# Performance work log

Hardware: AMD Instinct MI355X
Metric: run time of the kernel (lower is better)

Reference implementation:

```python
import jax, jax.numpy as jnp
import numpy as np

B, SQ, SP, H = 4, 2048, 2048, 256


def setup_inputs() -> dict:
    key = jax.random.key(0)
    k1, k2, k3 = jax.random.split(key, 3)
    return {
        "encode_input1": jax.random.normal(k1, (B, SQ, H), jnp.float32),  # E_q
        "encode_input2": jax.random.normal(k2, (B, SP, H), jnp.float32),  # E_p
        "input1_mask": jnp.ones((B, SP), jnp.float32),  # mask over seq_p (dim 1 of U)
        "input2_mask": jnp.ones((B, SQ), jnp.float32),  # mask over seq_q (dim 2 of U)
        "W": jax.random.normal(k3, (3 * H,), jnp.float32) * (1.0 / np.sqrt(3 * H)),
    }


def reference(encode_input1, encode_input2, input1_mask, input2_mask, W):
    E_q, E_p = encode_input1, encode_input2  # [B,q,H], [B,p,H]
    h = W.shape[0] // 3
    w_q, w_p, w_m = W[:h], W[h:2 * h], W[2 * h:]
    # Trilinear decomposition of Linear(cat([E_q, E_p, E_q*E_p])) -> [B,p,q]
    sq = E_q @ w_q                                   # [B,q]
    sp = E_p @ w_p                                   # [B,p]
    tri = jnp.einsum('bph,bqh->bpq', E_p * w_m, E_q)  # [B,p,q]
    U = sp[:, :, None] + sq[:, None, :] + tri
    mask = input1_mask[:, :, None] * input2_mask[:, None, :]  # [B,p,q]
    U = jnp.where(mask < 0.5, jnp.float32(-1e9), U)
    A_p = jax.nn.softmax(U, axis=2)  # softmax over q
    B_p = jax.nn.softmax(U, axis=1)  # softmax over p
    A1 = jnp.einsum('bpq,bqh->bph', A_p, E_q)  # A''_p  [B,p,H]
    B1 = jnp.einsum('bpq,bph->bqh', B_p, E_p)  # B''_p  [B,q,H]
    A2 = jnp.einsum('bpq,bqh->bph', A_p, B1)   # A'''_p [B,p,H]
    B2 = jnp.einsum('bpq,bph->bqh', B_p, A1)   # B'''_p [B,q,H]
    G_q_p = jnp.concatenate([E_p, A1, A2, E_p * A1, E_p * A2], axis=-1)  # [B,p,5H]
    G_p_q = jnp.concatenate([E_q, B1, B2, E_q * B1, E_q * B2], axis=-1)  # [B,q,5H]
    return (G_p_q, G_q_p)
```

## Files before the change

### kernel.cpp

```cpp
#include <hip/hip_runtime.h>
#include <math.h>

#define BB 4
#define SS 2048
#define HH 256
#define NEG_BIG -1e9f
#define GSEG ((size_t)BB * SS * 5 * HH)
#define NT ((size_t)BB * SS * HH)

typedef unsigned short ushort_t;
typedef __attribute__((ext_vector_type(8))) __bf16 bf16x8;
typedef __attribute__((ext_vector_type(8))) unsigned short ushort8;
typedef __attribute__((ext_vector_type(4))) float f32x4;

__device__ __forceinline__ void bsplit(float x, ushort_t& hi, ushort_t& lo) {
  union { float f; unsigned u; } a; a.f = x;
  unsigned r = a.u + 0x7FFFu + ((a.u >> 16) & 1u);
  ushort_t h = (ushort_t)(r >> 16);
  union { unsigned u; float f; } hf; hf.u = ((unsigned)h) << 16;
  float l = x - hf.f;
  union { float f; unsigned u; } b; b.f = l;
  unsigned r2 = b.u + 0x7FFFu + ((b.u >> 16) & 1u);
  hi = h; lo = (ushort_t)(r2 >> 16);
}

__global__ __launch_bounds__(256) void k_rowdots(
    const float* __restrict__ Eq, const float* __restrict__ Ep,
    const float* __restrict__ W,
    float* __restrict__ sqv, float* __restrict__ spv) {
  int g = blockIdx.x * 256 + threadIdx.x;
  int wid = g >> 6;
  int lane = g & 63;
  const int total = BB * SS;
  int isp = wid >= total;
  int row = isp ? (wid - total) : wid;
  const float* Er = (isp ? Ep : Eq) + (size_t)row * HH;
  const float* w = W + (isp ? HH : 0);
  float4 e = ((const float4*)Er)[lane];
  float4 wv = ((const float4*)w)[lane];
  float acc = e.x * wv.x + e.y * wv.y + e.z * wv.z + e.w * wv.w;
#pragma unroll
  for (int off = 32; off > 0; off >>= 1) acc += __shfl_down(acc, off, 64);
  if (lane == 0) (isp ? spv : sqv)[row] = acc;
}

__global__ __launch_bounds__(256) void k_tc(
    const float* __restrict__ src, ushort_t* __restrict__ dhi, ushort_t* __restrict__ dlo) {
  __shared__ float tile[64][65];
  int b = blockIdx.z;
  int r0 = blockIdx.x << 6;
  int h0 = blockIdx.y << 6;
  int tid = threadIdx.x;
  int rl = tid >> 4, c4 = (tid & 15) << 2;
  size_t srcb = (size_t)b * SS * HH;
#pragma unroll
  for (int i = 0; i < 4; ++i) {
    float4 v = *(const float4*)(src + srcb + (size_t)(r0 + rl + 16 * i) * HH + h0 + c4);
    tile[rl + 16 * i][c4 + 0] = v.x;
    tile[rl + 16 * i][c4 + 1] = v.y;
    tile[rl + 16 * i][c4 + 2] = v.z;
    tile[rl + 16 * i][c4 + 3] = v.w;
  }
  __syncthreads();
  size_t dstb = (size_t)b * HH;
#pragma unroll
  for (int i = 0; i < 4; ++i) {
    int h = rl + 16 * i;
    ushort4 h4, l4;
    ushort_t hh, ll;
    bsplit(tile[c4 + 0][h], hh, ll); h4.x = hh; l4.x = ll;
    bsplit(tile[c4 + 1][h], hh, ll); h4.y = hh; l4.y = ll;
    bsplit(tile[c4 + 2][h], hh, ll); h4.z = hh; l4.z = ll;
    bsplit(tile[c4 + 3][h], hh, ll); h4.w = hh; l4.w = ll;
    size_t o = (dstb + h0 + h) * SS + r0 + c4;
    *(ushort4*)(dhi + o) = h4;
    *(ushort4*)(dlo + o) = l4;
  }
}

__global__ __launch_bounds__(256) void k_tri(
    const float* __restrict__ Eq, const float* __restrict__ Ep,
    const float* __restrict__ W,
    const float* __restrict__ m1, const float* __restrict__ m2,
    const float* __restrict__ spv, const float* __restrict__ sqv,
    float* __restrict__ U) {
  alignas(16) __shared__ float As[32][68];
  alignas(16) __shared__ float Bs[32][68];
  int b = blockIdx.z;
  int q0 = blockIdx.x << 6;
  int p0 = blockIdx.y << 6;
  int tid = threadIdx.x;
  int tx = tid & 15, ty = tid >> 4;
  size_t bS = (size_t)b * SS;
  const float* EpB = Ep + bS * HH;
  const float* EqB = Eq + bS * HH;
  const float* wm = W + 2 * HH;
  float acc[4][4] = {};
  for (int k0 = 0; k0 < HH; k0 += 32) {
#pragma unroll
    for (int i = 0; i < 2; ++i) {
      int idx = tid + i * 256;
      int r = idx >> 3;
      int c4 = (idx & 7) << 2;
      float4 w4 = *(const float4*)(wm + k0 + c4);
      float4 a4 = *(const float4*)(EpB + (size_t)(p0 + r) * HH + k0 + c4);
      float4 b4 = *(const float4*)(EqB + (size_t)(q0 + r) * HH + k0 + c4);
      As[c4 + 0][r] = a4.x * w4.x;
      As[c4 + 1][r] = a4.y * w4.y;
      As[c4 + 2][r] = a4.z * w4.z;
      As[c4 + 3][r] = a4.w * w4.w;
      Bs[c4 + 0][r] = b4.x;
      Bs[c4 + 1][r] = b4.y;
      Bs[c4 + 2][r] = b4.z;
      Bs[c4 + 3][r] = b4.w;
    }
    __syncthreads();
#pragma unroll
    for (int k = 0; k < 32; ++k) {
      float4 a4 = *(const float4*)&As[k][ty << 2];
      float4 b4 = *(const float4*)&Bs[k][tx << 2];
      acc[0][0] += a4.x * b4.x; acc[0][1] += a4.x * b4.y; acc[0][2] += a4.x * b4.z; acc[0][3] += a4.x * b4.w;
      acc[1][0] += a4.y * b4.x; acc[1][1] += a4.y * b4.y; acc[1][2] += a4.y * b4.z; acc[1][3] += a4.y * b4.w;
      acc[2][0] += a4.z * b4.x; acc[2][1] += a4.z * b4.y; acc[2][2] += a4.z * b4.z; acc[2][3] += a4.z * b4.w;
      acc[3][0] += a4.w * b4.x; acc[3][1] += a4.w * b4.y; acc[3][2] += a4.w * b4.z; acc[3][3] += a4.w * b4.w;
    }
    __syncthreads();
  }
  int prow = p0 + (ty << 2);
  int qcol = q0 + (tx << 2);
  float spr[4], mpr[4], sqc[4], mqc[4];
#pragma unroll
  for (int i = 0; i < 4; ++i) { spr[i] = spv[bS + prow + i]; mpr[i] = m1[bS + prow + i]; }
#pragma unroll
  for (int j = 0; j < 4; ++j) { sqc[j] = sqv[bS + qcol + j]; mqc[j] = m2[bS + qcol + j]; }
#pragma unroll
  for (int i = 0; i < 4; ++i) {
    float4 o;
    o.x = (mpr[i] * mqc[0] < 0.5f) ? NEG_BIG : (acc[i][0] + spr[i] + sqc[0]);
    o.y = (mpr[i] * mqc[1] < 0.5f) ? NEG_BIG : (acc[i][1] + spr[i] + sqc[1]);
    o.z = (mpr[i] * mqc[2] < 0.5f) ? NEG_BIG : (acc[i][2] + spr[i] + sqc[2]);
    o.w = (mpr[i] * mqc[3] < 0.5f) ? NEG_BIG : (acc[i][3] + spr[i] + sqc[3]);
    *(float4*)(U + (bS + prow + i) * SS + qcol) = o;
  }
}

__global__ __launch_bounds__(256) void k_rowstats(
    const float* __restrict__ U, float* __restrict__ rowmax, float* __restrict__ rowinv) {
  __shared__ float redm[4];
  __shared__ float reds[4];
  int row = blockIdx.x;
  int tid = threadIdx.x;
  const float* u = U + (size_t)row * SS;
  float4 v1 = ((const float4*)u)[tid];
  float4 v2 = ((const float4*)u)[tid + 256];
  float m = fmaxf(fmaxf(fmaxf(v1.x, v1.y), fmaxf(v1.z, v1.w)),
                  fmaxf(fmaxf(v2.x, v2.y), fmaxf(v2.z, v2.w)));
#pragma unroll
  for (int off = 32; off > 0; off >>= 1) m = fmaxf(m, __shfl_down(m, off, 64));
  if ((tid & 63) == 0) redm[tid >> 6] = m;
  __syncthreads();
  m = fmaxf(fmaxf(redm[0], redm[1]), fmaxf(redm[2], redm[3]));
  float s = __expf(v1.x - m) + __expf(v1.y - m) + __expf(v1.z - m) + __expf(v1.w - m)
          + __expf(v2.x - m) + __expf(v2.y - m) + __expf(v2.z - m) + __expf(v2.w - m);
#pragma unroll
  for (int off = 32; off > 0; off >>= 1) s += __shfl_down(s, off, 64);
  if ((tid & 63) == 0) reds[tid >> 6] = s;
  __syncthreads();
  if (tid == 0) {
    float st = reds[0] + reds[1] + reds[2] + reds[3];
    rowmax[row] = m;
    rowinv[row] = 1.0f / st;
  }
}

__global__ __launch_bounds__(256) void k_colpart(
    const float* __restrict__ U, float* __restrict__ pm, float* __restrict__ ps) {
  int q = blockIdx.x * 256 + threadIdx.x;
  int pc = blockIdx.y;
  int b = blockIdx.z;
  const float* u = U + ((size_t)b * SS + pc * 128) * SS + q;
  float m = -INFINITY, s = 0.f;
  for (int p = 0; p < 128; ++p) {
    float x = u[(size_t)p * SS];
    float nm = fmaxf(m, x);
    s = s * __expf(m - nm) + __expf(x - nm);
    m = nm;
  }
  int o = (pc * BB + b) * SS + q;
  pm[o] = m;
  ps[o] = s;
}

__global__ __launch_bounds__(256) void k_colcomb(
    const float* __restrict__ pm, const float* __restrict__ ps,
    float* __restrict__ colmax, float* __restrict__ colinv) {
  int i = blockIdx.x * 256 + threadIdx.x;
  float m = -INFINITY;
#pragma unroll
  for (int pc = 0; pc < 16; ++pc) m = fmaxf(m, pm[(size_t)pc * BB * SS + i]);
  float s = 0.f;
#pragma unroll
  for (int pc = 0; pc < 16; ++pc)
    s += ps[(size_t)pc * BB * SS + i] * __expf(pm[(size_t)pc * BB * SS + i] - m);
  colmax[i] = m;
  colinv[i] = 1.0f / s;
}

template <int LEVEL>
__global__ __launch_bounds__(512, 4) void k_level(
    const float* __restrict__ U,
    const ushort_t* __restrict__ B0h, const ushort_t* __restrict__ B0l,
    const ushort_t* __restrict__ B1h, const ushort_t* __restrict__ B1l,
    const float* __restrict__ rowmax, const float* __restrict__ rowinv,
    const float* __restrict__ colmax, const float* __restrict__ colinv,
    const float* __restrict__ Eq, const float* __restrict__ Ep,
    float* __restrict__ A1w, float* __restrict__ B1w,
    float* __restrict__ out) {
  __shared__ ushort_t Ph[32 * 64];
  __shared__ ushort_t Pl[32 * 64];
  __shared__ ushort_t Bsh[256 * 64];
  __shared__ ushort_t Bsl[256 * 64];
  int b = blockIdx.z;
  int mode = blockIdx.y;
  int r0 = blockIdx.x << 5;
  int tid = threadIdx.x;
  size_t bS = (size_t)b * SS;
  const float* Ub = U + bS * SS;
  const ushort_t* Bh = (mode == 0 ? B0h : B1h) + (size_t)b * HH * SS;
  const ushort_t* Bl = (mode == 0 ? B0l : B1l) + (size_t)b * HH * SS;

  int srow0 = tid >> 4;
  int sc40 = (tid & 15) << 2;
  int srow1 = tid >> 3;
  int sc41 = (tid & 7) << 2;
  float rm = 0.f;
  float4 cm4;
  if (mode == 0) rm = rowmax[bS + r0 + srow0];
  else cm4 = *(const float4*)(colmax + bS + r0 + sc41);

  int w = tid >> 6, l = tid & 63;
  int wr = w >> 2, wc = w & 3;
  int arow = wr * 16 + (l & 15);
  unsigned asw = ((unsigned)(arow & 7)) << 4;
  int lk8 = (l >> 4) << 3;
  int hcol = wc * 64 + (l & 15);

  f32x4 acc[4];
#pragma unroll
  for (int i = 0; i < 4; ++i) acc[i] = (f32x4){0.f, 0.f, 0.f, 0.f};

  char* PhB = (char*)Ph;
  char* PlB = (char*)Pl;
  char* BhB = (char*)Bsh;
  char* BlB = (char*)Bsl;

  for (int k0 = 0; k0 < SS; k0 += 64) {
#pragma unroll
    for (int i = 0; i < 4; ++i) {
      int idx = tid + i * 512;
      int h = idx >> 3;
      int k8 = (idx & 7) << 3;
      unsigned off = ((unsigned)(h * 128 + k8 * 2)) ^ (((unsigned)(h & 7)) << 4);
      *(ushort8*)(BhB + off) = *(const ushort8*)(Bh + (size_t)h * SS + k0 + k8);
      *(ushort8*)(BlB + off) = *(const ushort8*)(Bl + (size_t)h * SS + k0 + k8);
    }
    if (mode == 0) {
      float4 u4 = *(const float4*)(Ub + (size_t)(r0 + srow0) * SS + k0 + sc40);
      ushort4 h4, l4;
      ushort_t hh, ll;
      bsplit(__expf(u4.x - rm), hh, ll); h4.x = hh; l4.x = ll;
      bsplit(__expf(u4.y - rm), hh, ll); h4.y = hh; l4.y = ll;
      bsplit(__expf(u4.z - rm), hh, ll); h4.z = hh; l4.z = ll;
      bsplit(__expf(u4.w - rm), hh, ll); h4.w = hh; l4.w = ll;
      unsigned off = ((unsigned)(srow0 * 128 + sc40 * 2)) ^ (((unsigned)(srow0 & 7)) << 4);
      *(ushort4*)(PhB + off) = h4;
      *(ushort4*)(PlB + off) = l4;
    } else {
      float4 u4 = *(const float4*)(Ub + (size_t)(k0 + srow1) * SS + r0 + sc41);
      float e[4] = {__expf(u4.x - cm4.x), __expf(u4.y - cm4.y),
                    __expf(u4.z - cm4.z), __expf(u4.w - cm4.w)};
#pragma unroll
      for (int j = 0; j < 4; ++j) {
        ushort_t hh, ll;
        bsplit(e[j], hh, ll);
        int rr = sc41 + j;
        unsigned off = ((unsigned)(rr * 128 + srow1 * 2)) ^ (((unsigned)(rr & 7)) << 4);
        *(ushort_t*)(PhB + off) = hh;
        *(ushort_t*)(PlB + off) = ll;
      }
    }
    __syncthreads();
#pragma unroll
    for (int kc = 0; kc < 64; kc += 32) {
      int ak = kc + lk8;
      unsigned aoff = ((unsigned)(arow * 128 + ak * 2)) ^ asw;
      bf16x8 ah = *(const bf16x8*)(PhB + aoff);
      bf16x8 al = *(const bf16x8*)(PlB + aoff);
#pragma unroll
      for (int cf = 0; cf < 4; ++cf) {
        int h = hcol + cf * 16;
        unsigned boff = ((unsigned)(h * 128 + ak * 2)) ^ (((unsigned)(h & 7)) << 4);
        bf16x8 bh = *(const bf16x8*)(BhB + boff);
        bf16x8 bl = *(const bf16x8*)(BlB + boff);
        acc[cf] = __builtin_amdgcn_mfma_f32_16x16x32_bf16(ah, bh, acc[cf], 0, 0, 0);
        acc[cf] = __builtin_amdgcn_mfma_f32_16x16x32_bf16(ah, bl, acc[cf], 0, 0, 0);
        acc[cf] = __builtin_amdgcn_mfma_f32_16x16x32_bf16(al, bh, acc[cf], 0, 0, 0);
      }
    }
    __syncthreads();
  }

  int crow = wr * 16 + ((l >> 4) << 2);
  if (LEVEL == 1) {
    const float* inv = mode == 0 ? rowinv : colinv;
    float* Out = mode == 0 ? A1w : B1w;
#pragma unroll
    for (int j = 0; j < 4; ++j) {
      int rr = r0 + crow + j;
      float sc = inv[bS + rr];
#pragma unroll
      for (int cf = 0; cf < 4; ++cf) {
        int h = hcol + cf * 16;
        Out[(bS + rr) * HH + h] = acc[cf][j] * sc;
      }
    }
  } else {
    if (mode == 0) {
      float* Gqp = out + GSEG;
#pragma unroll
      for (int j = 0; j < 4; ++j) {
        int rr = r0 + crow + j;
        float sc = rowinv[bS + rr];
#pragma unroll
        for (int cf = 0; cf < 4; ++cf) {
          int h = hcol + cf * 16;
          size_t eidx = (bS + rr) * HH + h;
          float a2 = acc[cf][j] * sc;
          float ep = Ep[eidx];
          float a1 = A1w[eidx];
          float* g = Gqp + (bS + rr) * (size_t)(5 * HH) + h;
          g[0 * HH] = ep;
          g[1 * HH] = a1;
          g[2 * HH] = a2;
          g[3 * HH] = ep * a1;
          g[4 * HH] = ep * a2;
        }
      }
    } else {
#pragma unroll
      for (int j = 0; j < 4; ++j) {
        int rr = r0 + crow + j;
        float sc = colinv[bS + rr];
#pragma unroll
        for (int cf = 0; cf < 4; ++cf) {
          int h = hcol + cf * 16;
          size_t eidx = (bS + rr) * HH + h;
          float b2 = acc[cf][j] * sc;
          float eq = Eq[eidx];
          float b1 = B1w[eidx];
          float* g = out + (bS + rr) * (size_t)(5 * HH) + h;
          g[0 * HH] = eq;
          g[1 * HH] = b1;
          g[2 * HH] = b2;
          g[3 * HH] = eq * b1;
          g[4 * HH] = eq * b2;
        }
      }
    }
  }
}

extern "C" void kernel_launch(void* const* d_in, const int* in_sizes, int n_in,
                              void* d_out, int out_size, void* d_ws, size_t ws_size,
                              hipStream_t stream) {
  const float* Eq = (const float*)d_in[0];
  const float* Ep = (const float*)d_in[1];
  const float* m1 = (const float*)d_in[2];
  const float* m2 = (const float*)d_in[3];
  const float* W  = (const float*)d_in[4];
  float* out = (float*)d_out;

  float* ws     = (float*)d_ws;
  float* U      = ws;
  float* rowmax = U + (size_t)BB * SS * SS;
  float* rowinv = rowmax + BB * SS;
  float* colmax = rowinv + BB * SS;
  float* colinv = colmax + BB * SS;
  float* spv    = colinv + BB * SS;
  float* sqv    = spv + BB * SS;
  float* A1w    = sqv + BB * SS;
  float* B1w    = A1w + NT;
  ushort_t* EqTh = (ushort_t*)(B1w + NT);
  ushort_t* EqTl = EqTh + NT;
  ushort_t* EpTh = EqTl + NT;
  ushort_t* EpTl = EpTh + NT;
  float* pm     = A1w;
  float* ps     = pm + 16 * BB * SS;
  ushort_t* A1Th = EqTh;
  ushort_t* A1Tl = EqTl;
  ushort_t* B1Th = EpTh;
  ushort_t* B1Tl = EpTl;

  dim3 tcg(SS / 64, HH / 64, BB);

  k_rowdots<<<2 * BB * SS / 4, 256, 0, stream>>>(Eq, Ep, W, sqv, spv);
  k_tc<<<tcg, 256, 0, stream>>>(Eq, EqTh, EqTl);
  k_tc<<<tcg, 256, 0, stream>>>(Ep, EpTh, EpTl);
  k_tri<<<dim3(SS / 64, SS / 64, BB), 256, 0, stream>>>(Eq, Ep, W, m1, m2, spv, sqv, U);
  k_rowstats<<<BB * SS, 256, 0, stream>>>(U, rowmax, rowinv);
  k_colpart<<<dim3(SS / 256, 16, BB), 256, 0, stream>>>(U, pm, ps);
  k_colcomb<<<BB * SS / 256, 256, 0, stream>>>(pm, ps, colmax, colinv);
  k_level<1><<<dim3(SS / 32, 2, BB), 512, 0, stream>>>(
      U, EqTh, EqTl, EpTh, EpTl, rowmax, rowinv, colmax, colinv,
      Eq, Ep, A1w, B1w, out);
  k_tc<<<tcg, 256, 0, stream>>>(A1w, A1Th, A1Tl);
  k_tc<<<tcg, 256, 0, stream>>>(B1w, B1Th, B1Tl);
  k_level<2><<<dim3(SS / 32, 2, BB), 512, 0, stream>>>(
      U, B1Th, B1Tl, A1Th, A1Tl, rowmax, rowinv, colmax, colinv,
      Eq, Ep, A1w, B1w, out);
}
```

Measured before the change: 425.9 us.

## Compute trilinear scores with split-bf16 MFMA instead of scalar FP32 FMA

Replaces the scalar FP32 tiled GEMM that builds U with an MFMA kernel fed by operands split into bf16 hi/lo parts (three-product emulation of FP32). Two new pre-pass kernels produce row-major hi/lo copies of Eq and of Ep scaled by w_m, stored in scratch buffers that are reused later. The intent is to move the 4x2048x2048x256 score GEMM onto matrix cores. In exchange it adds extra conversion passes and slightly reduced precision. The epilogue now writes U with scalar, uncoalesced-ish stores.

```diff
diff --git a/kernel.cpp b/kernel.cpp
--- a/kernel.cpp
+++ b/kernel.cpp
@@ -44,6 +44,33 @@
   if (lane == 0) (isp ? spv : sqv)[row] = acc;
 }
 
+__global__ __launch_bounds__(256) void k_rc(
+    const float* __restrict__ src, const float* __restrict__ wm,
+    ushort_t* __restrict__ dh, ushort_t* __restrict__ dl) {
+  size_t i = ((size_t)blockIdx.x * 256 + threadIdx.x) * 8;
+  float4 v0 = *(const float4*)(src + i);
+  float4 v1 = *(const float4*)(src + i + 4);
+  if (wm) {
+    int h = (int)(i & (HH - 1));
+    float4 w0 = *(const float4*)(wm + h);
+    float4 w1 = *(const float4*)(wm + h + 4);
+    v0.x *= w0.x; v0.y *= w0.y; v0.z *= w0.z; v0.w *= w0.w;
+    v1.x *= w1.x; v1.y *= w1.y; v1.z *= w1.z; v1.w *= w1.w;
+  }
+  ushort8 h8, l8;
+  ushort_t hh, ll;
+  bsplit(v0.x, hh, ll); h8[0] = hh; l8[0] = ll;
+  bsplit(v0.y, hh, ll); h8[1] = hh; l8[1] = ll;
+  bsplit(v0.z, hh, ll); h8[2] = hh; l8[2] = ll;
+  bsplit(v0.w, hh, ll); h8[3] = hh; l8[3] = ll;
+  bsplit(v1.x, hh, ll); h8[4] = hh; l8[4] = ll;
+  bsplit(v1.y, hh, ll); h8[5] = hh; l8[5] = ll;
+  bsplit(v1.z, hh, ll); h8[6] = hh; l8[6] = ll;
+  bsplit(v1.w, hh, ll); h8[7] = hh; l8[7] = ll;
+  *(ushort8*)(dh + i) = h8;
+  *(ushort8*)(dl + i) = l8;
+}
+
 __global__ __launch_bounds__(256) void k_tc(
     const float* __restrict__ src, ushort_t* __restrict__ dhi, ushort_t* __restrict__ dlo) {
   __shared__ float tile[64][65];
@@ -78,69 +105,97 @@
   }
 }
 
-__global__ __launch_bounds__(256) void k_tri(
-    const float* __restrict__ Eq, const float* __restrict__ Ep,
-    const float* __restrict__ W,
+__global__ __launch_bounds__(512, 4) void k_trim(
+    const ushort_t* __restrict__ Ah_g, const ushort_t* __restrict__ Al_g,
+    const ushort_t* __restrict__ Bh_g, const ushort_t* __restrict__ Bl_g,
     const float* __restrict__ m1, const float* __restrict__ m2,
     const float* __restrict__ spv, const float* __restrict__ sqv,
     float* __restrict__ U) {
-  alignas(16) __shared__ float As[32][68];
-  alignas(16) __shared__ float Bs[32][68];
+  __shared__ ushort_t Ash[32 * 64];
+  __shared__ ushort_t Asl[32 * 64];
+  __shared__ ushort_t Bsh[256 * 64];
+  __shared__ ushort_t Bsl[256 * 64];
   int b = blockIdx.z;
-  int q0 = blockIdx.x << 6;
-  int p0 = blockIdx.y << 6;
+  int q0 = blockIdx.x << 8;
+  int p0 = blockIdx.y << 5;
   int tid = threadIdx.x;
-  int tx = tid & 15, ty = tid >> 4;
   size_t bS = (size_t)b * SS;
-  const float* EpB = Ep + bS * HH;
-  const float* EqB = Eq + bS * HH;
-  const float* wm = W + 2 * HH;
-  float acc[4][4] = {};
-  for (int k0 = 0; k0 < HH; k0 += 32) {
-#pragma unroll
-    for (int i = 0; i < 2; ++i) {
-      int idx = tid + i * 256;
-      int r = idx >> 3;
-      int c4 = (idx & 7) << 2;
-      float4 w4 = *(const float4*)(wm + k0 + c4);
-      float4 a4 = *(const float4*)(EpB + (size_t)(p0 + r) * HH + k0 + c4);
-      float4 b4 = *(const float4*)(EqB + (size_t)(q0 + r) * HH + k0 + c4);
-      As[c4 + 0][r] = a4.x * w4.x;
-      As[c4 + 1][r] = a4.y * w4.y;
-      As[c4 + 2][r] = a4.z * w4.z;
-      As[c4 + 3][r] = a4.w * w4.w;
-      Bs[c4 + 0][r] = b4.x;
-      Bs[c4 + 1][r] = b4.y;
-      Bs[c4 + 2][r] = b4.z;
-      Bs[c4 + 3][r] = b4.w;
+
+  int w = tid >> 6, l = tid & 63;
+  int wr = w >> 2, wc = w & 3;
+  int arow = wr * 16 + (l & 15);
+  unsigned asw = ((unsigned)(arow & 7)) << 4;
+  int lk8 = (l >> 4) << 3;
+  int qcl = wc * 64 + (l & 15);
+
+  f32x4 acc[4];
+#pragma unroll
+  for (int i = 0; i < 4; ++i) acc[i] = (f32x4){0.f, 0.f, 0.f, 0.f};
+
+  char* AshB = (char*)Ash;
+  char* AslB = (char*)Asl;
+  char* BshB = (char*)Bsh;
+  char* BslB = (char*)Bsl;
+
+  for (int k0 = 0; k0 < HH; k0 += 64) {
+    if (tid < 256) {
+      int row = tid >> 3;
+      int k8 = (tid & 7) << 3;
+      unsigned off = ((unsigned)(row * 128 + k8 * 2)) ^ (((unsigned)(row & 7)) << 4);
+      size_t g = (bS + p0 + row) * HH + k0 + k8;
+      *(ushort8*)(AshB + off) = *(const ushort8*)(Ah_g + g);
+      *(ushort8*)(AslB + off) = *(const ushort8*)(Al_g + g);
+    }
+#pragma unroll
+    for (int i = 0; i < 4; ++i) {
+      int idx = tid + i * 512;
+      int row = idx >> 3;
+      int k8 = (idx & 7) << 3;
+      unsigned off = ((unsigned)(row * 128 + k8 * 2)) ^ (((unsigned)(row & 7)) << 4);
+      size_t g = (bS + q0 + row) * HH + k0 + k8;
+      *(ushort8*)(BshB + off) = *(const ushort8*)(Bh_g + g);
+      *(ushort8*)(BslB + off) = *(const ushort8*)(Bl_g + g);
     }
     __syncthreads();
 #pragma unroll
-    for (int k = 0; k < 32; ++k) {
-      float4 a4 = *(const float4*)&As[k][ty << 2];
-      float4 b4 = *(const float4*)&Bs[k][tx << 2];
-      acc[0][0] += a4.x * b4.x; acc[0][1] += a4.x * b4.y; acc[0][2] += a4.x * b4.z; acc[0][3] += a4.x * b4.w;
-      acc[1][0] += a4.y * b4.x; acc[1][1] += a4.y * b4.y; acc[1][2] += a4.y * b4.z; acc[1][3] += a4.y * b4.w;
-      acc[2][0] += a4.z * b4.x; acc[2][1] += a4.z * b4.y; acc[2][2] += a4.z * b4.z; acc[2][3] += a4.z * b4.w;
-      acc[3][0] += a4.w * b4.x; acc[3][1] += a4.w * b4.y; acc[3][2] += a4.w * b4.z; acc[3][3] += a4.w * b4.w;
+    for (int kc = 0; kc < 64; kc += 32) {
+      int ak = kc + lk8;
+      unsigned aoff = ((unsigned)(arow * 128 + ak * 2)) ^ asw;
+      bf16x8 ah = *(const bf16x8*)(AshB + aoff);
+      bf16x8 al = *(const bf16x8*)(AslB + aoff);
+#pragma unroll
+      for (int cf = 0; cf < 4; ++cf) {
+        int r = qcl + cf * 16;
+        unsigned boff = ((unsigned)(r * 128 + ak * 2)) ^ (((unsigned)(r & 7)) << 4);
+        bf16x8 bh = *(const bf16x8*)(BshB + boff);
+        bf16x8 bl = *(const bf16x8*)(BslB + boff);
+        acc[cf] = __builtin_amdgcn_mfma_f32_16x16x32_bf16(ah, bh, acc[cf], 0, 0, 0);
+        acc[cf] = __builtin_amdgcn_mfma_f32_16x16x32_bf16(ah, bl, acc[cf], 0, 0, 0);
+        acc[cf] = __builtin_amdgcn_mfma_f32_16x16x32_bf16(al, bh, acc[cf], 0, 0, 0);
+      }
     }
     __syncthreads();
   }
-  int prow = p0 + (ty << 2);
-  int qcol = q0 + (tx << 2);
-  float spr[4], mpr[4], sqc[4], mqc[4];
-#pragma unroll
-  for (int i = 0; i < 4; ++i) { spr[i] = spv[bS + prow + i]; mpr[i] = m1[bS + prow + i]; }
-#pragma unroll
-  for (int j = 0; j < 4; ++j) { sqc[j] = sqv[bS + qcol + j]; mqc[j] = m2[bS + qcol + j]; }
-#pragma unroll
-  for (int i = 0; i < 4; ++i) {
-    float4 o;
-    o.x = (mpr[i] * mqc[0] < 0.5f) ? NEG_BIG : (acc[i][0] + spr[i] + sqc[0]);
-    o.y = (mpr[i] * mqc[1] < 0.5f) ? NEG_BIG : (acc[i][1] + spr[i] + sqc[1]);
-    o.z = (mpr[i] * mqc[2] < 0.5f) ? NEG_BIG : (acc[i][2] + spr[i] + sqc[2]);
-    o.w = (mpr[i] * mqc[3] < 0.5f) ? NEG_BIG : (acc[i][3] + spr[i] + sqc[3]);
-    *(float4*)(U + (bS + prow + i) * SS + qcol) = o;
+
+  int crow = wr * 16 + ((l >> 4) << 2);
+  float spr[4], mpr[4];
+#pragma unroll
+  for (int j = 0; j < 4; ++j) {
+    spr[j] = spv[bS + p0 + crow + j];
+    mpr[j] = m1[bS + p0 + crow + j];
+  }
+#pragma unroll
+  for (int cf = 0; cf < 4; ++cf) {
+    int q = q0 + qcl + cf * 16;
+    float sqc = sqv[bS + q];
+    float mqc = m2[bS + q];
+#pragma unroll
+    for (int j = 0; j < 4; ++j) {
+      int p = p0 + crow + j;
+      float v = acc[cf][j] + spr[j] + sqc;
+      if (mpr[j] * mqc < 0.5f) v = NEG_BIG;
+      U[(bS + p) * SS + q] = v;
+    }
   }
 }
 
@@ -394,6 +449,10 @@
   ushort_t* EqTl = EqTh + NT;
   ushort_t* EpTh = EqTl + NT;
   ushort_t* EpTl = EpTh + NT;
+  ushort_t* EqRh = (ushort_t*)A1w;
+  ushort_t* EqRl = EqRh + NT;
+  ushort_t* ApRh = (ushort_t*)B1w;
+  ushort_t* ApRl = ApRh + NT;
   float* pm     = A1w;
   float* ps     = pm + 16 * BB * SS;
   ushort_t* A1Th = EqTh;
@@ -404,9 +463,12 @@
   dim3 tcg(SS / 64, HH / 64, BB);
 
   k_rowdots<<<2 * BB * SS / 4, 256, 0, stream>>>(Eq, Ep, W, sqv, spv);
+  k_rc<<<(int)(NT / 2048), 256, 0, stream>>>(Eq, nullptr, EqRh, EqRl);
+  k_rc<<<(int)(NT / 2048), 256, 0, stream>>>(Ep, W + 2 * HH, ApRh, ApRl);
   k_tc<<<tcg, 256, 0, stream>>>(Eq, EqTh, EqTl);
   k_tc<<<tcg, 256, 0, stream>>>(Ep, EpTh, EpTl);
-  k_tri<<<dim3(SS / 64, SS / 64, BB), 256, 0, stream>>>(Eq, Ep, W, m1, m2, spv, sqv, U);
+  k_trim<<<dim3(SS / 256, SS / 32, BB), 512, 0, stream>>>(
+      ApRh, ApRl, EqRh, EqRl, m1, m2, spv, sqv, U);
   k_rowstats<<<BB * SS, 256, 0, stream>>>(U, rowmax, rowinv);
   k_colpart<<<dim3(SS / 256, 16, BB), 256, 0, stream>>>(U, pm, ps);
   k_colcomb<<<BB * SS / 256, 256, 0, stream>>>(pm, ps, colmax, colinv);
```

New measurement: 358.7 us. 1.19x faster.
